# Kernel optimization log

Hardware: AMD Instinct MI355X
Metric: run time of the kernel (lower is better)

## Reference

```python
import jax, jax.numpy as jnp
import numpy as np

BQ, BP, L, CIN, H1, H2, COUT = 32, 256, 16, 8192, 256, 32, 8192


def _conv_block(x, w1, b1, w2, b2, w3, b3):
    # x: (B, L, H1) -> Conv1d stack over token dim with residual, as in self.convs
    h = jnp.transpose(x, (0, 2, 1))  # (B, H1, L)
    for w, b in ((w1, b1), (w2, b2), (w3, b3)):
        h = jax.lax.conv_general_dilated(h, w, (1,), [(2, 2)],
                                         dimension_numbers=('NCH', 'OIH', 'NCH'))
        h = jax.nn.relu(h + b[None, :, None])
    return jnp.transpose(h, (0, 2, 1)) + x


def setup_inputs() -> dict:
    key = jax.random.key(0)
    ks = jax.random.split(key, 16)
    query_x = (jax.random.uniform(ks[0], (BQ, L, CIN)) < 0.01).astype(jnp.float32)
    poi_x = (jax.random.uniform(ks[1], (BP, L, CIN)) < 0.01).astype(jnp.float32)
    query_loc = jax.random.uniform(ks[2], (BQ, 2)) * 100.0
    poi_loc = jax.random.uniform(ks[3], (BP, 2)) * 100.0
    enc_w = jax.random.normal(ks[4], (H1, CIN)) * 0.02
    conv_w1 = jax.random.normal(ks[5], (H1, H1, 5)) * 0.02
    conv_w2 = jax.random.normal(ks[6], (H1, H1, 5)) * 0.02
    conv_w3 = jax.random.normal(ks[7], (H1, H1, 5)) * 0.02
    conv_b1 = jnp.zeros((H1,), jnp.float32)
    conv_b2 = jnp.zeros((H1,), jnp.float32)
    conv_b3 = jnp.zeros((H1,), jnp.float32)
    dec_w1 = jax.random.normal(ks[8], (H2, 2 * H1)) * 0.05
    dec_b1 = jnp.zeros((H2,), jnp.float32)
    dec_w2 = jax.random.normal(ks[9], (H2, H2)) * 0.1
    dec_b2 = jnp.zeros((H2,), jnp.float32)
    # torch init fills this with 0; use small randn so the path is non-trivial
    dec_w3 = jax.random.normal(ks[10], (COUT, H2)) * 0.01
    a = jnp.asarray(1.0, jnp.float32)
    b = jnp.asarray(0.0, jnp.float32)
    c = jnp.asarray(1.0, jnp.float32)
    d = jnp.asarray(0.0, jnp.float32)
    return dict(query_x=query_x, query_loc=query_loc, poi_x=poi_x, poi_loc=poi_loc,
                enc_w=enc_w, conv_w1=conv_w1, conv_b1=conv_b1, conv_w2=conv_w2,
                conv_b2=conv_b2, conv_w3=conv_w3, conv_b3=conv_b3,
                dec_w1=dec_w1, dec_b1=dec_b1, dec_w2=dec_w2, dec_b2=dec_b2,
                dec_w3=dec_w3, a=a, b=b, c=c, d=d)


def reference(query_x, query_loc, poi_x, poi_loc, enc_w, conv_w1, conv_b1,
              conv_w2, conv_b2, conv_w3, conv_b3, dec_w1, dec_b1, dec_w2,
              dec_b2, dec_w3, a, b, c, d):
    # --- encode ---
    q_h = _conv_block(query_x @ enc_w.T, conv_w1, conv_b1, conv_w2, conv_b2, conv_w3, conv_b3)
    p_h = _conv_block(poi_x @ enc_w.T, conv_w1, conv_b1, conv_w2, conv_b2, conv_w3, conv_b3)
    q_emb = q_h.mean(axis=1)  # (Bq, H1)
    p_emb = p_h.mean(axis=1)  # (Bp, H1)
    # --- bloom masks ---
    q_bloom = jnp.minimum(query_x.sum(axis=1), 1.0)  # (Bq, 8192)
    p_bloom = jnp.minimum(poi_x.sum(axis=1), 1.0)    # (Bp, 8192)
    interaction = q_bloom[:, None, :] * p_bloom[None, :, :]  # (Bq, Bp, 8192)
    q_bits = q_bloom.sum(axis=-1, keepdims=True)             # (Bq, 1)
    # --- pairwise MLP decode ---
    bq, bp = q_emb.shape[0], p_emb.shape[0]
    all_embed = jnp.concatenate([
        jnp.broadcast_to(q_emb[:, None, :], (bq, bp, q_emb.shape[-1])),
        jnp.broadcast_to(p_emb[None, :, :], (bq, bp, p_emb.shape[-1])),
    ], axis=-1)  # (Bq, Bp, 2*H1)
    h = jax.nn.relu(all_embed)
    h = jax.nn.relu(h @ dec_w1.T + dec_b1)
    h = jax.nn.relu(h @ dec_w2.T + dec_b2)
    w = h @ dec_w3.T  # (Bq, Bp, 8192)
    weights = jnp.where(w >= 0, w, w * 0.125) + 1.0  # LeakyReLU(1/8) + 1
    desc_sim = (interaction * weights).sum(axis=-1) / q_bits  # (Bq, Bp)
    # --- geo-distance fusion ---
    dist = jnp.sqrt(((query_loc[:, None, :] - poi_loc[None, :, :]) ** 2).sum(axis=-1))
    mean = desc_sim.mean(axis=-1, keepdims=True)
    std = jnp.std(desc_sim, axis=-1, keepdims=True, ddof=1)  # torch.std is unbiased
    desc_sim = (desc_sim - mean) / (std + 1e-6)
    dist_sim = -jnp.log(dist + 1.0)
    return (c - jax.nn.sigmoid(a * desc_sim + b)) * (dist_sim - d)
```

## Files before the change

### kernel.cpp

```cpp
#include <hip/hip_runtime.h>

#define NB 288
#define NBQ 32
#define NBP 256
#define LTOK 16
#define CIN 8192
#define H1 256
#define H2 32
#define MASKW 256
#define XROW 264

typedef __attribute__((ext_vector_type(8))) short short8;
typedef __attribute__((ext_vector_type(4))) float f32x4;

__device__ __forceinline__ unsigned short f2bf(float f) {
    unsigned u = __float_as_uint(f);
    u += 0x7fffu + ((u >> 16) & 1u);
    return (unsigned short)(u >> 16);
}
__device__ __forceinline__ float bf2f(unsigned short u) {
    return __uint_as_float(((unsigned)u) << 16);
}

__global__ __launch_bounds__(256) void k_prep(const float* __restrict__ encw,
                                              const float* __restrict__ w1,
                                              const float* __restrict__ w2,
                                              const float* __restrict__ w3c,
                                              const float* __restrict__ dw3,
                                              unsigned* __restrict__ wtp,
                                              unsigned short* __restrict__ wtb,
                                              unsigned* __restrict__ w3p,
                                              unsigned* __restrict__ masks,
                                              float* __restrict__ Cmat) {
    int g = blockIdx.x, tid = threadIdx.x;
    if (g < 2048) {
        __shared__ float tile[32][33];
        int k0 = (g >> 3) * 32, h0 = (g & 7) * 32;
        int tx = tid & 31, ty = tid >> 5;
#pragma unroll
        for (int i = 0; i < 32; i += 8)
            tile[ty + i][tx] = encw[(h0 + ty + i) * CIN + k0 + tx];
        __syncthreads();
        int kl = tid >> 3, pw = tid & 7;
#pragma unroll
        for (int u = 0; u < 2; ++u) {
            int p = pw + u * 8;
            unsigned lo = f2bf(tile[2 * p][kl]);
            unsigned hi = f2bf(tile[2 * p + 1][kl]);
            wtp[(size_t)(k0 + kl) * 128 + (h0 >> 1) + p] = (hi << 16) | lo;
        }
    } else if (g < 5888) {
        int bx = g - 2048;
        int l = bx / 1280;
        int r = bx - l * 1280;
        int o = r / 5;
        int d = r - o * 5;
        const float* w = (l == 0) ? w1 : (l == 1) ? w2 : w3c;
        wtb[(size_t)l * 327680 + (size_t)o * 1280 + d * 256 + tid] =
            f2bf(w[(size_t)o * 1280 + tid * 5 + d]);
    } else if (g < 6400) {
        int idx = (g - 5888) * 256 + tid;
        int k = idx >> 4, pw = idx & 15;
        unsigned lo = f2bf(dw3[k * 32 + 2 * pw]);
        unsigned hi = f2bf(dw3[k * 32 + 2 * pw + 1]);
        w3p[idx] = (hi << 16) | lo;
    } else {
        int b = g - 6400;
        masks[b * MASKW + tid] = 0u;
        if (tid < 32) Cmat[b * 32 + tid] = 0.f;
        if (b == 0 && tid < 128) wtp[(size_t)8192 * 128 + tid] = 0u;
    }
}

__global__ __launch_bounds__(256) void k_scanG(const float* __restrict__ qx,
                                               const float* __restrict__ px,
                                               const unsigned* __restrict__ wtp,
                                               unsigned* __restrict__ masks,
                                               unsigned* __restrict__ xbufu) {
    int row = blockIdx.x;
    int b = row >> 4;
    const float* x = (b < NBQ) ? (qx + (size_t)row * CIN)
                               : (px + (size_t)(row - NBQ * LTOK) * CIN);
    __shared__ int idxs[200];
    __shared__ int cnt;
    __shared__ float sL[2][128], sH[2][128];
    int tid = threadIdx.x;
    if (tid == 0) cnt = 0;
    __syncthreads();
    const float4* x4 = (const float4*)x;
    float4 r[8];
#pragma unroll
    for (int j = 0; j < 8; ++j) r[j] = x4[j * 256 + tid];
#pragma unroll
    for (int j = 0; j < 8; ++j) {
        unsigned ox = __float_as_uint(r[j].x) | __float_as_uint(r[j].y) |
                      __float_as_uint(r[j].z) | __float_as_uint(r[j].w);
        if (ox) {
            int base = (j * 256 + tid) * 4;
            float vv[4] = {r[j].x, r[j].y, r[j].z, r[j].w};
#pragma unroll
            for (int c = 0; c < 4; ++c) {
                if (vv[c] != 0.f) {
                    int k = base + c;
                    int p = atomicAdd(&cnt, 1);
                    if (p < 192) idxs[p] = k;
                    atomicOr(&masks[b * MASKW + (k >> 5)], 1u << (k & 31));
                }
            }
        }
    }
    __syncthreads();
    int n = min(cnt, 192);
    for (int i = n + tid; i < 200; i += 256) idxs[i] = 8192;
    __syncthreads();
    int pair = tid & 127, half = tid >> 7;
    float aL = 0.f, aH = 0.f;
    for (int j0 = 0; j0 < n; j0 += 8) {
        int4 ia = *(const int4*)(idxs + j0 + half * 4);
        int id[4] = {ia.x, ia.y, ia.z, ia.w};
#pragma unroll
        for (int u = 0; u < 4; ++u) {
            unsigned v = wtp[(size_t)id[u] * 128 + pair];
            aL += __uint_as_float(v << 16);
            aH += __uint_as_float(v & 0xffff0000u);
        }
    }
    sL[half][pair] = aL; sH[half][pair] = aH;
    __syncthreads();
    if (tid < 128) {
        float L = sL[0][tid] + sL[1][tid];
        float H = sH[0][tid] + sH[1][tid];
        unsigned bl = f2bf(L), bh = f2bf(H);
        xbufu[(size_t)row * 128 + tid] = (bh << 16) | bl;
    }
}

__global__ __launch_bounds__(256) void k_cgemm(const unsigned short* __restrict__ actIn,
                                               unsigned short* __restrict__ actOut,
                                               const unsigned short* __restrict__ wl,
                                               const float* __restrict__ bias) {
    __shared__ unsigned short Als[2 * 20 * XROW];
    int tid = threadIdx.x;
    int m0 = blockIdx.x * 32, n0 = blockIdx.y * 32;

    int row = tid >> 3, part = tid & 7;
    {
        const short8* src = (const short8*)(actIn + (size_t)(m0 + row) * 256 + part * 32);
        unsigned short* dst = Als + ((row >> 4) * 20 + (row & 15) + 2) * XROW + part * 32;
#pragma unroll
        for (int j = 0; j < 4; ++j) *(short8*)(dst + j * 8) = src[j];
    }
    if (tid < 132) {
        int* Az = (int*)Als;
#pragma unroll
        for (int pr = 0; pr < 8; ++pr) {
            const int rr[8] = {0, 1, 18, 19, 20, 21, 38, 39};
            Az[rr[pr] * 132 + tid] = 0;
        }
    }

    int lane = tid & 63, wave = tid >> 6;
    int lane15 = lane & 15, quad = lane >> 4;
    int wm = wave & 1, wn = wave >> 1;
    const unsigned short* bsrc = wl + (size_t)(n0 + wn * 16 + lane15) * 1280 + quad * 8;
    __syncthreads();

    f32x4 acc = (f32x4){0.f, 0.f, 0.f, 0.f};
#pragma unroll
    for (int d = 0; d < 5; ++d) {
        short8 bv[8];
#pragma unroll
        for (int kk = 0; kk < 8; ++kk)
            bv[kk] = *(const short8*)(bsrc + d * 256 + kk * 32);
        const unsigned short* ap = Als + (wm * 20 + lane15 + d) * XROW + quad * 8;
#pragma unroll
        for (int kk = 0; kk < 8; ++kk) {
            short8 av = *(const short8*)(ap + kk * 32);
            acc = __builtin_amdgcn_mfma_f32_16x16x32_bf16(av, bv[kk], acc, 0, 0, 0);
        }
    }

    int o = n0 + wn * 16 + lane15;
    float bvv = bias[o];
    int rbase = m0 + wm * 16 + quad * 4;
#pragma unroll
    for (int r = 0; r < 4; ++r)
        actOut[(size_t)(rbase + r) * 256 + o] = f2bf(fmaxf(acc[r] + bvv, 0.f));
}

__global__ __launch_bounds__(256) void k_cgemm3(const unsigned short* __restrict__ actIn,
                                                const unsigned short* __restrict__ wl,
                                                const float* __restrict__ bias,
                                                const unsigned short* __restrict__ xbuf,
                                                const float* __restrict__ dw1,
                                                float* __restrict__ Cmat) {
    __shared__ unsigned short Als[2 * 20 * XROW];
    __shared__ float els[2][32];
    int tid = threadIdx.x;
    int m0 = blockIdx.x * 32, n0 = blockIdx.y * 32;

    int row = tid >> 3, part = tid & 7;
    {
        const short8* src = (const short8*)(actIn + (size_t)(m0 + row) * 256 + part * 32);
        unsigned short* dst = Als + ((row >> 4) * 20 + (row & 15) + 2) * XROW + part * 32;
#pragma unroll
        for (int j = 0; j < 4; ++j) *(short8*)(dst + j * 8) = src[j];
    }
    if (tid < 132) {
        int* Az = (int*)Als;
#pragma unroll
        for (int pr = 0; pr < 8; ++pr) {
            const int rr[8] = {0, 1, 18, 19, 20, 21, 38, 39};
            Az[rr[pr] * 132 + tid] = 0;
        }
    }

    int lane = tid & 63, wave = tid >> 6;
    int lane15 = lane & 15, quad = lane >> 4;
    int wm = wave & 1, wn = wave >> 1;
    const unsigned short* bsrc = wl + (size_t)(n0 + wn * 16 + lane15) * 1280 + quad * 8;
    __syncthreads();

    f32x4 acc = (f32x4){0.f, 0.f, 0.f, 0.f};
#pragma unroll
    for (int d = 0; d < 5; ++d) {
        short8 bv[8];
#pragma unroll
        for (int kk = 0; kk < 8; ++kk)
            bv[kk] = *(const short8*)(bsrc + d * 256 + kk * 32);
        const unsigned short* ap = Als + (wm * 20 + lane15 + d) * XROW + quad * 8;
#pragma unroll
        for (int kk = 0; kk < 8; ++kk) {
            short8 av = *(const short8*)(ap + kk * 32);
            acc = __builtin_amdgcn_mfma_f32_16x16x32_bf16(av, bv[kk], acc, 0, 0, 0);
        }
    }

    int o_l = wn * 16 + lane15;
    int o = n0 + o_l;
    float bvv = bias[o];
    float sf = 0.f;
#pragma unroll
    for (int r = 0; r < 4; ++r) sf += fmaxf(acc[r] + bvv, 0.f);
    sf += __shfl_xor(sf, 16, 64);
    sf += __shfl_xor(sf, 32, 64);
    if (quad == 0) {
        int bb = 2 * blockIdx.x + wm;
        float rs = 0.f;
#pragma unroll
        for (int t = 0; t < 16; ++t)
            rs += bf2f(xbuf[((size_t)bb * 16 + t) * 256 + o]);
        els[wm][o_l] = fmaxf((sf + rs) * (1.f / 16.f), 0.f);
    }
    __syncthreads();
    if (tid < 64) {
        int b2 = tid >> 5, op = tid & 31;
        int bb = 2 * blockIdx.x + b2;
        const float* wr = dw1 + (size_t)op * 512 + (bb < NBQ ? 0 : 256) + n0;
        float s = 0.f;
#pragma unroll
        for (int j = 0; j < 32; ++j) s = fmaf(wr[j], els[b2][j], s);
        atomicAdd(&Cmat[bb * 32 + op], s);
    }
}

__global__ __launch_bounds__(256) void k_pair(const float* __restrict__ Cmat,
                                              const float* __restrict__ b1,
                                              const float* __restrict__ w2,
                                              const float* __restrict__ b2,
                                              const unsigned* __restrict__ w3p,
                                              const unsigned* __restrict__ masks,
                                              float* __restrict__ desc) {
    int p = blockIdx.x, q = blockIdx.y;
    __shared__ float h1[32];
    __shared__ __align__(16) float h2s[32];
    __shared__ int idxs[3072];
    __shared__ int cnt;
    __shared__ float wsum[4], wq[4];
    int tid = threadIdx.x;
    if (tid == 0) cnt = 0;
    __syncthreads();
    unsigned mq = masks[q * MASKW + tid];
    unsigned m = mq & masks[(NBQ + p) * MASKW + tid];
    int nb = __popc(m);
    if (nb) {
        int pos = atomicAdd(&cnt, nb);
        while (m) {
            int bit = __ffs(m) - 1;
            m &= m - 1;
            idxs[pos++] = tid * 32 + bit;
        }
    }
    if (tid < 32)
        h1[tid] = fmaxf(Cmat[q * 32 + tid] + Cmat[(NBQ + p) * 32 + tid] + b1[tid], 0.f);
    __syncthreads();
    if (tid < 32) {
        float s = b2[tid];
#pragma unroll
        for (int j = 0; j < 32; ++j) s = fmaf(w2[tid * 32 + j], h1[j], s);
        h2s[tid] = fmaxf(s, 0.f);
    }
    __syncthreads();
    int n = cnt;
    int rowi = tid >> 2, part = tid & 3;
    float h2v[8];
#pragma unroll
    for (int j = 0; j < 8; ++j) h2v[j] = h2s[part * 8 + j];
    float local = 0.f;
    if (n > 0) {
        bool act = rowi < n;
        uint4 wv = *(const uint4*)(w3p + (size_t)idxs[act ? rowi : 0] * 16 + part * 4);
        for (int base = 0; base < n; base += 64) {
            int rn = base + 64 + rowi;
            bool actn = rn < n;
            uint4 nv = *(const uint4*)(w3p + (size_t)idxs[actn ? rn : 0] * 16 + part * 4);
            float dot = 0.f;
            unsigned wu[4] = {wv.x, wv.y, wv.z, wv.w};
#pragma unroll
            for (int u = 0; u < 4; ++u) {
                dot += __uint_as_float(wu[u] << 16) * h2v[2 * u];
                dot += __uint_as_float(wu[u] & 0xffff0000u) * h2v[2 * u + 1];
            }
            dot += __shfl_xor(dot, 1);
            dot += __shfl_xor(dot, 2);
            if (act && part == 0)
                local += 1.f + (dot >= 0.f ? dot : dot * 0.125f);
            wv = nv;
            act = actn;
        }
    }
    float qcf = (float)__popc(mq);
#pragma unroll
    for (int st = 1; st < 64; st <<= 1) {
        local += __shfl_xor(local, st);
        qcf   += __shfl_xor(qcf, st);
    }
    if ((tid & 63) == 0) { wsum[tid >> 6] = local; wq[tid >> 6] = qcf; }
    __syncthreads();
    if (tid == 0) {
        float t  = wsum[0] + wsum[1] + wsum[2] + wsum[3];
        float qb = wq[0] + wq[1] + wq[2] + wq[3];
        desc[q * 256 + p] = t / qb;
    }
}

__global__ __launch_bounds__(256) void k_final(const float* __restrict__ desc,
                                               const float* __restrict__ qloc,
                                               const float* __restrict__ ploc,
                                               const float* __restrict__ sa,
                                               const float* __restrict__ sb,
                                               const float* __restrict__ sc,
                                               const float* __restrict__ sd,
                                               float* __restrict__ out) {
    __shared__ float red[256];
    int q = blockIdx.x, tid = threadIdx.x;
    float v = desc[q * 256 + tid];
    red[tid] = v; __syncthreads();
    for (int st = 128; st > 0; st >>= 1) {
        if (tid < st) red[tid] += red[tid + st];
        __syncthreads();
    }
    float mean = red[0] * (1.f / 256.f);
    __syncthreads();
    float dv = v - mean;
    red[tid] = dv * dv; __syncthreads();
    for (int st = 128; st > 0; st >>= 1) {
        if (tid < st) red[tid] += red[tid + st];
        __syncthreads();
    }
    float var = red[0] * (1.f / 255.f);
    float norm = dv / (sqrtf(var) + 1e-6f);
    float dx = qloc[q * 2]     - ploc[tid * 2];
    float dy = qloc[q * 2 + 1] - ploc[tid * 2 + 1];
    float dist = sqrtf(dx * dx + dy * dy);
    float z = sa[0] * norm + sb[0];
    float sig = 1.f / (1.f + expf(-z));
    out[q * 256 + tid] = (sc[0] - sig) * (-logf(dist + 1.f) - sd[0]);
}

extern "C" void kernel_launch(void* const* d_in, const int* in_sizes, int n_in,
                              void* d_out, int out_size, void* d_ws, size_t ws_size,
                              hipStream_t stream) {
    const float* qx   = (const float*)d_in[0];
    const float* qloc = (const float*)d_in[1];
    const float* px   = (const float*)d_in[2];
    const float* ploc = (const float*)d_in[3];
    const float* encw = (const float*)d_in[4];
    const float* cw1  = (const float*)d_in[5];
    const float* cb1  = (const float*)d_in[6];
    const float* cw2  = (const float*)d_in[7];
    const float* cb2  = (const float*)d_in[8];
    const float* cw3  = (const float*)d_in[9];
    const float* cb3  = (const float*)d_in[10];
    const float* dw1  = (const float*)d_in[11];
    const float* db1  = (const float*)d_in[12];
    const float* dw2  = (const float*)d_in[13];
    const float* db2  = (const float*)d_in[14];
    const float* dw3  = (const float*)d_in[15];
    const float* sa   = (const float*)d_in[16];
    const float* sb   = (const float*)d_in[17];
    const float* sc   = (const float*)d_in[18];
    const float* sd   = (const float*)d_in[19];

    char* w = (char*)d_ws;
    unsigned*       wtp   = (unsigned*)w;       w += (size_t)8193 * 128 * 4;
    unsigned short* xbuf  = (unsigned short*)w; w += (size_t)NB * LTOK * H1 * 2;
    unsigned short* act1  = (unsigned short*)w; w += (size_t)NB * LTOK * H1 * 2;
    unsigned short* act2  = (unsigned short*)w; w += (size_t)NB * LTOK * H1 * 2;
    unsigned short* wtb   = (unsigned short*)w; w += (size_t)3 * 256 * 1280 * 2;
    unsigned*       w3p   = (unsigned*)w;       w += (size_t)CIN * 16 * 4;
    float*          Cmat  = (float*)w;          w += (size_t)NB * H2 * 4;
    unsigned*       masks = (unsigned*)w;       w += (size_t)NB * MASKW * 4;
    float*          desc  = (float*)w;          w += (size_t)NBQ * NBP * 4;

    k_prep<<<6688, 256, 0, stream>>>(encw, cw1, cw2, cw3, dw3,
                                     wtp, wtb, w3p, masks, Cmat);
    k_scanG<<<NB * LTOK, 256, 0, stream>>>(qx, px, wtp, masks, (unsigned*)xbuf);
    dim3 cgrid(NB * LTOK / 32, 8);
    k_cgemm<<<cgrid, 256, 0, stream>>>(xbuf, act1, wtb,          cb1);
    k_cgemm<<<cgrid, 256, 0, stream>>>(act1, act2, wtb + 327680, cb2);
    k_cgemm3<<<cgrid, 256, 0, stream>>>(act2, wtb + 2 * 327680, cb3, xbuf, dw1, Cmat);
    k_pair<<<dim3(NBP, NBQ), 256, 0, stream>>>(Cmat, db1, dw2, db2, w3p, masks, desc);
    k_final<<<NBQ, 256, 0, stream>>>(desc, qloc, ploc, sa, sb, sc, sd, (float*)d_out);
}
```

Before: 362.8 us.

## Fuse three conv layers into one per-sample kernel with activations in LDS

After: 398.5 us. +9.9%, slower.

```diff
diff --git a/kernel.cpp b/kernel.cpp
--- a/kernel.cpp
+++ b/kernel.cpp
@@ -30,8 +30,7 @@
                                               unsigned* __restrict__ wtp,
                                               unsigned short* __restrict__ wtb,
                                               unsigned* __restrict__ w3p,
-                                              unsigned* __restrict__ masks,
-                                              float* __restrict__ Cmat) {
+                                              unsigned* __restrict__ masks) {
     int g = blockIdx.x, tid = threadIdx.x;
     if (g < 2048) {
         __shared__ float tile[32][33];
@@ -67,7 +66,6 @@
     } else {
         int b = g - 6400;
         masks[b * MASKW + tid] = 0u;
-        if (tid < 32) Cmat[b * 32 + tid] = 0.f;
         if (b == 0 && tid < 128) wtp[(size_t)8192 * 128 + tid] = 0u;
     }
 }
@@ -135,132 +133,115 @@
     }
 }
 
-__global__ __launch_bounds__(256) void k_cgemm(const unsigned short* __restrict__ actIn,
-                                               unsigned short* __restrict__ actOut,
-                                               const unsigned short* __restrict__ wl,
-                                               const float* __restrict__ bias) {
-    __shared__ unsigned short Als[2 * 20 * XROW];
+__device__ __forceinline__ void conv_strip(const unsigned short* __restrict__ Ac,
+                                           const unsigned short* __restrict__ wl,
+                                           int lane15, int quad, int n0,
+                                           f32x4& acc0, f32x4& acc1) {
+    acc0 = (f32x4){0.f, 0.f, 0.f, 0.f};
+    acc1 = (f32x4){0.f, 0.f, 0.f, 0.f};
+#pragma unroll
+    for (int d = 0; d < 5; ++d) {
+        const unsigned short* ap = Ac + (lane15 + d) * XROW + quad * 8;
+        short8 av[8];
+#pragma unroll
+        for (int kk = 0; kk < 8; ++kk) av[kk] = *(const short8*)(ap + kk * 32);
+        const unsigned short* bp0 = wl + (size_t)(n0 + lane15) * 1280 + d * 256 + quad * 8;
+        const unsigned short* bp1 = bp0 + 16 * 1280;
+#pragma unroll
+        for (int kk = 0; kk < 8; ++kk) {
+            short8 bv0 = *(const short8*)(bp0 + kk * 32);
+            acc0 = __builtin_amdgcn_mfma_f32_16x16x32_bf16(av[kk], bv0, acc0, 0, 0, 0);
+            short8 bv1 = *(const short8*)(bp1 + kk * 32);
+            acc1 = __builtin_amdgcn_mfma_f32_16x16x32_bf16(av[kk], bv1, acc1, 0, 0, 0);
+        }
+    }
+}
+
+__global__ __launch_bounds__(512) void k_conv(const unsigned short* __restrict__ xbuf,
+                                              const unsigned short* __restrict__ wtb,
+                                              const float* __restrict__ cb1,
+                                              const float* __restrict__ cb2,
+                                              const float* __restrict__ cb3,
+                                              const float* __restrict__ dw1,
+                                              float* __restrict__ Cmat) {
+    __shared__ unsigned short A0[20 * XROW];
+    __shared__ unsigned short A1[20 * XROW];
+    __shared__ float ecol[256];
+    __shared__ float xsum[256];
+    int b = blockIdx.x;
     int tid = threadIdx.x;
-    int m0 = blockIdx.x * 32, n0 = blockIdx.y * 32;
-
-    int row = tid >> 3, part = tid & 7;
+
     {
-        const short8* src = (const short8*)(actIn + (size_t)(m0 + row) * 256 + part * 32);
-        unsigned short* dst = Als + ((row >> 4) * 20 + (row & 15) + 2) * XROW + part * 32;
-#pragma unroll
-        for (int j = 0; j < 4; ++j) *(short8*)(dst + j * 8) = src[j];
+        int row = tid >> 5, part = tid & 31;
+        *(short8*)(A0 + (row + 2) * XROW + part * 8) =
+            *(const short8*)(xbuf + ((size_t)b * 16 + row) * 256 + part * 8);
     }
     if (tid < 132) {
-        int* Az = (int*)Als;
-#pragma unroll
-        for (int pr = 0; pr < 8; ++pr) {
-            const int rr[8] = {0, 1, 18, 19, 20, 21, 38, 39};
-            Az[rr[pr] * 132 + tid] = 0;
-        }
+        int* a0 = (int*)A0; int* a1 = (int*)A1;
+        a0[tid] = 0; a0[132 + tid] = 0; a0[18 * 132 + tid] = 0; a0[19 * 132 + tid] = 0;
+        a1[tid] = 0; a1[132 + tid] = 0; a1[18 * 132 + tid] = 0; a1[19 * 132 + tid] = 0;
+    }
+    __syncthreads();
+    if (tid < 256) {
+        float s = 0.f;
+#pragma unroll
+        for (int t = 0; t < 16; ++t) s += bf2f(A0[(t + 2) * XROW + tid]);
+        xsum[tid] = s;
     }
 
     int lane = tid & 63, wave = tid >> 6;
     int lane15 = lane & 15, quad = lane >> 4;
-    int wm = wave & 1, wn = wave >> 1;
-    const unsigned short* bsrc = wl + (size_t)(n0 + wn * 16 + lane15) * 1280 + quad * 8;
-    __syncthreads();
-
-    f32x4 acc = (f32x4){0.f, 0.f, 0.f, 0.f};
-#pragma unroll
-    for (int d = 0; d < 5; ++d) {
-        short8 bv[8];
-#pragma unroll
-        for (int kk = 0; kk < 8; ++kk)
-            bv[kk] = *(const short8*)(bsrc + d * 256 + kk * 32);
-        const unsigned short* ap = Als + (wm * 20 + lane15 + d) * XROW + quad * 8;
-#pragma unroll
-        for (int kk = 0; kk < 8; ++kk) {
-            short8 av = *(const short8*)(ap + kk * 32);
-            acc = __builtin_amdgcn_mfma_f32_16x16x32_bf16(av, bv[kk], acc, 0, 0, 0);
-        }
-    }
-
-    int o = n0 + wn * 16 + lane15;
-    float bvv = bias[o];
-    int rbase = m0 + wm * 16 + quad * 4;
-#pragma unroll
-    for (int r = 0; r < 4; ++r)
-        actOut[(size_t)(rbase + r) * 256 + o] = f2bf(fmaxf(acc[r] + bvv, 0.f));
-}
-
-__global__ __launch_bounds__(256) void k_cgemm3(const unsigned short* __restrict__ actIn,
-                                                const unsigned short* __restrict__ wl,
-                                                const float* __restrict__ bias,
-                                                const unsigned short* __restrict__ xbuf,
-                                                const float* __restrict__ dw1,
-                                                float* __restrict__ Cmat) {
-    __shared__ unsigned short Als[2 * 20 * XROW];
-    __shared__ float els[2][32];
-    int tid = threadIdx.x;
-    int m0 = blockIdx.x * 32, n0 = blockIdx.y * 32;
-
-    int row = tid >> 3, part = tid & 7;
+    int n0 = wave * 32;
+    f32x4 acc0, acc1;
+
+    conv_strip(A0, wtb, lane15, quad, n0, acc0, acc1);
     {
-        const short8* src = (const short8*)(actIn + (size_t)(m0 + row) * 256 + part * 32);
-        unsigned short* dst = Als + ((row >> 4) * 20 + (row & 15) + 2) * XROW + part * 32;
-#pragma unroll
-        for (int j = 0; j < 4; ++j) *(short8*)(dst + j * 8) = src[j];
-    }
-    if (tid < 132) {
-        int* Az = (int*)Als;
-#pragma unroll
-        for (int pr = 0; pr < 8; ++pr) {
-            const int rr[8] = {0, 1, 18, 19, 20, 21, 38, 39};
-            Az[rr[pr] * 132 + tid] = 0;
-        }
-    }
-
-    int lane = tid & 63, wave = tid >> 6;
-    int lane15 = lane & 15, quad = lane >> 4;
-    int wm = wave & 1, wn = wave >> 1;
-    const unsigned short* bsrc = wl + (size_t)(n0 + wn * 16 + lane15) * 1280 + quad * 8;
-    __syncthreads();
-
-    f32x4 acc = (f32x4){0.f, 0.f, 0.f, 0.f};
-#pragma unroll
-    for (int d = 0; d < 5; ++d) {
-        short8 bv[8];
-#pragma unroll
-        for (int kk = 0; kk < 8; ++kk)
-            bv[kk] = *(const short8*)(bsrc + d * 256 + kk * 32);
-        const unsigned short* ap = Als + (wm * 20 + lane15 + d) * XROW + quad * 8;
-#pragma unroll
-        for (int kk = 0; kk < 8; ++kk) {
-            short8 av = *(const short8*)(ap + kk * 32);
-            acc = __builtin_amdgcn_mfma_f32_16x16x32_bf16(av, bv[kk], acc, 0, 0, 0);
-        }
-    }
-
-    int o_l = wn * 16 + lane15;
-    int o = n0 + o_l;
-    float bvv = bias[o];
-    float sf = 0.f;
-#pragma unroll
-    for (int r = 0; r < 4; ++r) sf += fmaxf(acc[r] + bvv, 0.f);
-    sf += __shfl_xor(sf, 16, 64);
-    sf += __shfl_xor(sf, 32, 64);
-    if (quad == 0) {
-        int bb = 2 * blockIdx.x + wm;
-        float rs = 0.f;
-#pragma unroll
-        for (int t = 0; t < 16; ++t)
-            rs += bf2f(xbuf[((size_t)bb * 16 + t) * 256 + o]);
-        els[wm][o_l] = fmaxf((sf + rs) * (1.f / 16.f), 0.f);
-    }
-    __syncthreads();
-    if (tid < 64) {
-        int b2 = tid >> 5, op = tid & 31;
-        int bb = 2 * blockIdx.x + b2;
-        const float* wr = dw1 + (size_t)op * 512 + (bb < NBQ ? 0 : 256) + n0;
+        float bv0 = cb1[n0 + lane15], bv1 = cb1[n0 + 16 + lane15];
+#pragma unroll
+        for (int r = 0; r < 4; ++r) {
+            A1[(2 + quad * 4 + r) * XROW + n0 + lane15]      = f2bf(fmaxf(acc0[r] + bv0, 0.f));
+            A1[(2 + quad * 4 + r) * XROW + n0 + 16 + lane15] = f2bf(fmaxf(acc1[r] + bv1, 0.f));
+        }
+    }
+    __syncthreads();
+
+    conv_strip(A1, wtb + 327680, lane15, quad, n0, acc0, acc1);
+    {
+        float bv0 = cb2[n0 + lane15], bv1 = cb2[n0 + 16 + lane15];
+#pragma unroll
+        for (int r = 0; r < 4; ++r) {
+            A0[(2 + quad * 4 + r) * XROW + n0 + lane15]      = f2bf(fmaxf(acc0[r] + bv0, 0.f));
+            A0[(2 + quad * 4 + r) * XROW + n0 + 16 + lane15] = f2bf(fmaxf(acc1[r] + bv1, 0.f));
+        }
+    }
+    __syncthreads();
+
+    conv_strip(A0, wtb + 2 * 327680, lane15, quad, n0, acc0, acc1);
+    {
+        float bv0 = cb3[n0 + lane15], bv1 = cb3[n0 + 16 + lane15];
+        float s0 = 0.f, s1 = 0.f;
+#pragma unroll
+        for (int r = 0; r < 4; ++r) {
+            s0 += fmaxf(acc0[r] + bv0, 0.f);
+            s1 += fmaxf(acc1[r] + bv1, 0.f);
+        }
+        s0 += __shfl_xor(s0, 16, 64); s0 += __shfl_xor(s0, 32, 64);
+        s1 += __shfl_xor(s1, 16, 64); s1 += __shfl_xor(s1, 32, 64);
+        if (quad == 0) {
+            ecol[n0 + lane15]      = s0;
+            ecol[n0 + 16 + lane15] = s1;
+        }
+    }
+    __syncthreads();
+    if (tid < 256)
+        ecol[tid] = fmaxf((ecol[tid] + xsum[tid]) * (1.f / 16.f), 0.f);
+    __syncthreads();
+    if (tid < 32) {
+        const float* wr = dw1 + (size_t)tid * 512 + (b < NBQ ? 0 : 256);
         float s = 0.f;
-#pragma unroll
-        for (int j = 0; j < 32; ++j) s = fmaf(wr[j], els[b2][j], s);
-        atomicAdd(&Cmat[bb * 32 + op], s);
+#pragma unroll 8
+        for (int j = 0; j < 256; ++j) s = fmaf(wr[j], ecol[j], s);
+        Cmat[b * 32 + tid] = s;
     }
 }
 
@@ -307,27 +288,23 @@
 #pragma unroll
     for (int j = 0; j < 8; ++j) h2v[j] = h2s[part * 8 + j];
     float local = 0.f;
-    if (n > 0) {
-        bool act = rowi < n;
-        uint4 wv = *(const uint4*)(w3p + (size_t)idxs[act ? rowi : 0] * 16 + part * 4);
-        for (int base = 0; base < n; base += 64) {
-            int rn = base + 64 + rowi;
-            bool actn = rn < n;
-            uint4 nv = *(const uint4*)(w3p + (size_t)idxs[actn ? rn : 0] * 16 + part * 4);
-            float dot = 0.f;
+    for (int base = 0; base < n; base += 64) {
+        int r = base + rowi;
+        bool act = r < n;
+        float dot = 0.f;
+        if (act) {
+            uint4 wv = *(const uint4*)(w3p + (size_t)idxs[r] * 16 + part * 4);
             unsigned wu[4] = {wv.x, wv.y, wv.z, wv.w};
 #pragma unroll
             for (int u = 0; u < 4; ++u) {
                 dot += __uint_as_float(wu[u] << 16) * h2v[2 * u];
                 dot += __uint_as_float(wu[u] & 0xffff0000u) * h2v[2 * u + 1];
             }
-            dot += __shfl_xor(dot, 1);
-            dot += __shfl_xor(dot, 2);
-            if (act && part == 0)
-                local += 1.f + (dot >= 0.f ? dot : dot * 0.125f);
-            wv = nv;
-            act = actn;
-        }
+        }
+        dot += __shfl_xor(dot, 1);
+        dot += __shfl_xor(dot, 2);
+        if (act && part == 0)
+            local += 1.f + (dot >= 0.f ? dot : dot * 0.125f);
     }
     float qcf = (float)__popc(mq);
 #pragma unroll
@@ -405,21 +382,15 @@
     char* w = (char*)d_ws;
     unsigned*       wtp   = (unsigned*)w;       w += (size_t)8193 * 128 * 4;
     unsigned short* xbuf  = (unsigned short*)w; w += (size_t)NB * LTOK * H1 * 2;
-    unsigned short* act1  = (unsigned short*)w; w += (size_t)NB * LTOK * H1 * 2;
-    unsigned short* act2  = (unsigned short*)w; w += (size_t)NB * LTOK * H1 * 2;
     unsigned short* wtb   = (unsigned short*)w; w += (size_t)3 * 256 * 1280 * 2;
     unsigned*       w3p   = (unsigned*)w;       w += (size_t)CIN * 16 * 4;
     float*          Cmat  = (float*)w;          w += (size_t)NB * H2 * 4;
     unsigned*       masks = (unsigned*)w;       w += (size_t)NB * MASKW * 4;
     float*          desc  = (float*)w;          w += (size_t)NBQ * NBP * 4;
 
-    k_prep<<<6688, 256, 0, stream>>>(encw, cw1, cw2, cw3, dw3,
-                                     wtp, wtb, w3p, masks, Cmat);
+    k_prep<<<6688, 256, 0, stream>>>(encw, cw1, cw2, cw3, dw3, wtp, wtb, w3p, masks);
     k_scanG<<<NB * LTOK, 256, 0, stream>>>(qx, px, wtp, masks, (unsigned*)xbuf);
-    dim3 cgrid(NB * LTOK / 32, 8);
-    k_cgemm<<<cgrid, 256, 0, stream>>>(xbuf, act1, wtb,          cb1);
-    k_cgemm<<<cgrid, 256, 0, stream>>>(act1, act2, wtb + 327680, cb2);
-    k_cgemm3<<<cgrid, 256, 0, stream>>>(act2, wtb + 2 * 327680, cb3, xbuf, dw1, Cmat);
+    k_conv<<<NB, 512, 0, stream>>>(xbuf, wtb, cb1, cb2, cb3, dw1, Cmat);
     k_pair<<<dim3(NBP, NBQ), 256, 0, stream>>>(Cmat, db1, dw2, db2, w3p, masks, desc);
     k_final<<<NBQ, 256, 0, stream>>>(desc, qloc, ploc, sa, sb, sc, sd, (float*)d_out);
 }
```
